# Optimization experiments

Measured on AMD Instinct MI355X. Metric: run time of the kernel, lower is better.

Reference implementation:

```python
import jax, jax.numpy as jnp
import numpy as np

N_NEIGHBORS = 16
NEIGHBOR_LIMIT = 20
N_BINS = 5
EPS = 1e-12


def _distance_matrix(coords):
    # coords: (N, 3) -> (N, N) pairwise Euclidean distances
    sq = jnp.sum(coords * coords, axis=-1)
    dm = sq[:, None] - 2.0 * (coords @ coords.T) + sq[None, :]
    return jnp.sqrt(jnp.abs(dm))


def _shot_lrf(nbh, radius):
    # nbh: (N, K, 3) local neighbor coordinates. SHOT local reference frames.
    d = jnp.linalg.norm(nbh, axis=-1)                       # (N, K)
    w = jnp.maximum(radius - d, 0.0)                        # SHOT distance weights
    cov = jnp.einsum("nk,nki,nkj->nij", w, nbh, nbh)
    cov = cov / (jnp.sum(w, axis=-1)[:, None, None] + EPS)  # (N, 3, 3)
    _, eigvecs = jnp.linalg.eigh(cov)                       # ascending eigenvalues
    x_axes = eigvecs[:, :, 2]                               # largest eigenvalue
    z_axes = eigvecs[:, :, 0]                               # smallest eigenvalue (normal)

    def disambiguate(axes):
        dots = jnp.einsum("nki,ni->nk", nbh, axes)
        pos = jnp.sum((dots >= 0.0).astype(jnp.float32), axis=-1)
        neg = jnp.sum((dots < 0.0).astype(jnp.float32), axis=-1)
        sign = jnp.where(pos >= neg, 1.0, -1.0)
        return axes * sign[:, None]

    x_axes = disambiguate(x_axes)
    z_axes = disambiguate(z_axes)
    y_axes = jnp.cross(z_axes, x_axes)
    return jnp.stack([x_axes, y_axes, z_axes], axis=1)      # (N, 3, 3)


def _log_map(lrfs, nbh):
    # project local neighbors onto tangent plane, preserving vector length
    u = jnp.einsum("nki,ni->nk", nbh, lrfs[:, 0])
    v = jnp.einsum("nki,ni->nk", nbh, lrfs[:, 1])
    plane = jnp.stack([u, v], axis=-1)                      # (N, K, 2)
    norms = jnp.linalg.norm(nbh, axis=-1)
    plane_norms = jnp.linalg.norm(plane, axis=-1)
    return plane * (norms / (plane_norms + EPS))[..., None]


def _histograms(proj, radius, n_bins):
    # proj: (N, K, 2) tangent-plane projections -> (N, n_bins**2) normalized histograms
    step = 2.0 * radius / n_bins
    c = jnp.linspace(-radius, radius, n_bins + 1)[:-1] + step / 2.0
    weights = radius - jnp.sqrt(c[:, None] ** 2 + c[None, :] ** 2)  # (n_bins, n_bins)

    bins = jnp.floor((proj + radius) / step)                # (N, K, 2)
    valid = jnp.all((bins >= 0.0) & (bins < n_bins), axis=-1)
    bx = jnp.clip(bins[..., 0].astype(jnp.int32), 0, n_bins - 1)
    by = jnp.clip(bins[..., 1].astype(jnp.int32), 0, n_bins - 1)
    flat = by * n_bins + bx                                 # hist[row=y_bin, col=x_bin]
    n_pts = flat.shape[0]
    b2 = n_bins * n_bins
    offset = jnp.arange(n_pts)[:, None] * b2
    hist = jnp.zeros((n_pts * b2,), jnp.float32).at[(offset + flat).reshape(-1)].add(
        valid.reshape(-1).astype(jnp.float32))
    hist = hist.reshape(n_pts, n_bins, n_bins) * weights[None]
    hist = hist / jnp.linalg.norm(hist, axis=(1, 2), keepdims=True)
    return hist.reshape(n_pts, b2)


def _single_cloud(coords):
    dm = _distance_matrix(coords)
    order = jnp.argsort(dm, axis=-1)
    dsort = jnp.take_along_axis(dm, order, axis=-1)
    radius = jnp.mean(dsort[:, N_NEIGHBORS])
    nbr_idx = order[:, :NEIGHBOR_LIMIT]
    nbr_dist = dsort[:, :NEIGHBOR_LIMIT]
    nbh = coords[nbr_idx] - coords[:, None, :]              # (N, K, 3) local coords
    fill = (2.0 * radius) / jnp.sqrt(3.0)                   # dummy coord of length 2*radius
    nbh = jnp.where((nbr_dist > radius)[..., None], fill, nbh)
    lrfs = _shot_lrf(nbh, radius)
    proj = _log_map(lrfs, nbh)
    return _histograms(proj, radius, N_BINS)


def setup_inputs() -> dict:
    key = jax.random.key(0)
    batched_coordinates = jax.random.normal(key, (4, 4096, 3), dtype=jnp.float32)
    return {"batched_coordinates": batched_coordinates}


def reference(batched_coordinates):
    return jax.vmap(_single_cloud)(batched_coordinates)
```

## Files before the change

### kernel.cpp

```cpp
#include <hip/hip_runtime.h>
#include <math.h>

#pragma clang fp contract(off)

#define NPTS 4096
#define NBATCH 4
#define NTOT (NBATCH * NPTS)
#define NNB 20
#define NBINS 5
#define LTOP 7

#define SEPS    5.9604644775390625e-8f
#define SSAFMIN 1.17549435e-38f


__device__ __forceinline__ float f_signf(float a, float b) {
  return __builtin_signbit(b) ? -fabsf(a) : fabsf(a);
}

__device__ float slapy2_(float x, float y) {
  float xa = fabsf(x), ya = fabsf(y);
  float w = fmaxf(xa, ya), z = fminf(xa, ya);
  if (z == 0.0f) return w;
  float t = z / w;
  return w * sqrtf(1.0f + t * t);
}

__device__ void slartg_(float f, float g, float* c, float* s, float* r) {
  if (g == 0.0f) {
    *c = 1.0f; *s = 0.0f; *r = f;
  } else if (f == 0.0f) {
    *c = 0.0f; *s = __builtin_signbit(g) ? -1.0f : 1.0f; *r = fabsf(g);
  } else {
    float f1 = fabsf(f);
    float d = sqrtf(f * f + g * g);
    *c = f1 / d;
    float rr = __builtin_signbit(f) ? -d : d;
    *r = rr;
    *s = g / rr;
  }
}

__device__ void slaev2_(float a, float b, float c,
                        float* rt1, float* rt2, float* cs1, float* sn1) {
  float sm = a + c;
  float df = a - c;
  float adf = fabsf(df);
  float tb = b + b;
  float ab = fabsf(tb);
  float acmx, acmn;
  if (fabsf(a) > fabsf(c)) { acmx = a; acmn = c; } else { acmx = c; acmn = a; }
  float rt;
  if (adf > ab)      { float t = ab / adf; rt = adf * sqrtf(1.0f + t * t); }
  else if (adf < ab) { float t = adf / ab; rt = ab * sqrtf(1.0f + t * t); }
  else               { rt = ab * sqrtf(2.0f); }
  int sgn1;
  if (sm < 0.0f) {
    *rt1 = 0.5f * (sm - rt); sgn1 = -1;
    *rt2 = (acmx / *rt1) * acmn - (b / *rt1) * b;
  } else if (sm > 0.0f) {
    *rt1 = 0.5f * (sm + rt); sgn1 = 1;
    *rt2 = (acmx / *rt1) * acmn - (b / *rt1) * b;
  } else {
    *rt1 = 0.5f * rt; *rt2 = -0.5f * rt; sgn1 = 1;
  }
  float cs; int sgn2;
  if (df >= 0.0f) { cs = df + rt; sgn2 = 1; }
  else            { cs = df - rt; sgn2 = -1; }
  float acs = fabsf(cs);
  float csv, snv;
  if (acs > ab) {
    float ct = -tb / cs;
    snv = 1.0f / sqrtf(1.0f + ct * ct);
    csv = ct * snv;
  } else {
    if (ab == 0.0f) { csv = 1.0f; snv = 0.0f; }
    else {
      float tn = -cs / tb;
      csv = 1.0f / sqrtf(1.0f + tn * tn);
      snv = tn * csv;
    }
  }
  if (sgn1 == sgn2) { float tn = csv; csv = -snv; snv = tn; }
  *cs1 = csv; *sn1 = snv;
}

__device__ __forceinline__ float sel3(float a0, float a1, float a2, int i) {
  float r = (i == 1) ? a1 : a0;
  return (i == 2) ? a2 : r;
}
__device__ __forceinline__ float sel2(float a0, float a1, int i) {
  return (i == 1) ? a1 : a0;
}
#define RD(i)   sel3(d0, d1, d2, (i))
#define RE(i)   sel2(e0, e1, (i))
#define RC(i)   sel2(c0r, c1r, (i))
#define RS(i)   sel2(s0r, s1r, (i))
#define WD(i,v) do{ float _t=(v); int _i=(i); d0=(_i==0)?_t:d0; d1=(_i==1)?_t:d1; d2=(_i==2)?_t:d2; }while(0)
#define WE(i,v) do{ float _t=(v); int _i=(i); e0=(_i==0)?_t:e0; e1=(_i==1)?_t:e1; }while(0)
#define WC(i,v) do{ float _t=(v); int _i=(i); c0r=(_i==0)?_t:c0r; c1r=(_i==1)?_t:c1r; }while(0)
#define WS(i,v) do{ float _t=(v); int _i=(i); s0r=(_i==0)?_t:s0r; s1r=(_i==1)?_t:s1r; }while(0)
#define ZROT(ja, jb, cc, ss) do{ int _a=(ja), _b=(jb); float _c=(cc), _s=(ss);                       \
  { float ta=sel3(z00,z01,z02,_a), tb=sel3(z00,z01,z02,_b); float na=_c*ta-_s*tb, nb=_s*ta+_c*tb;   \
    z00=(_a==0)?na:((_b==0)?nb:z00); z01=(_a==1)?na:((_b==1)?nb:z01); z02=(_a==2)?na:((_b==2)?nb:z02);} \
  { float ta=sel3(z10,z11,z12,_a), tb=sel3(z10,z11,z12,_b); float na=_c*ta-_s*tb, nb=_s*ta+_c*tb;   \
    z10=(_a==0)?na:((_b==0)?nb:z10); z11=(_a==1)?na:((_b==1)?nb:z11); z12=(_a==2)?na:((_b==2)?nb:z12);} \
  { float ta=sel3(z20,z21,z22,_a), tb=sel3(z20,z21,z22,_b); float na=_c*ta-_s*tb, nb=_s*ta+_c*tb;   \
    z20=(_a==0)?na:((_b==0)?nb:z20); z21=(_a==1)?na:((_b==1)?nb:z21); z22=(_a==2)?na:((_b==2)?nb:z22);} \
}while(0)
#define ZSWAP(ia, ib) do{ int _a=(ia), _b=(ib);                                                     \
  { float ta=sel3(z00,z01,z02,_a), tb=sel3(z00,z01,z02,_b);                                         \
    z00=(_a==0)?tb:((_b==0)?ta:z00); z01=(_a==1)?tb:((_b==1)?ta:z01); z02=(_a==2)?tb:((_b==2)?ta:z02);} \
  { float ta=sel3(z10,z11,z12,_a), tb=sel3(z10,z11,z12,_b);                                         \
    z10=(_a==0)?tb:((_b==0)?ta:z10); z11=(_a==1)?tb:((_b==1)?ta:z11); z12=(_a==2)?tb:((_b==2)?ta:z12);} \
  { float ta=sel3(z20,z21,z22,_a), tb=sel3(z20,z21,z22,_b);                                         \
    z20=(_a==0)?tb:((_b==0)?ta:z20); z21=(_a==1)?tb:((_b==1)?ta:z21); z22=(_a==2)?tb:((_b==2)?ta:z22);} \
}while(0)

__device__ void eigh3f_reg(float A00, float A10, float A20, float A11, float A21, float A22,
                           float V[3][3]) {
  float taui, v2, beta;
  float alpha = A10;
  float xnorm = fabsf(A20);
  if (xnorm == 0.0f) {
    taui = 0.0f; beta = alpha; v2 = 0.0f;
  } else {
    beta = -f_signf(slapy2_(alpha, xnorm), alpha);
    taui = (beta - alpha) / beta;
    v2 = A20 * (1.0f / (alpha - beta));
  }
  float a11 = A11, a21 = A21, a22 = A22;
  if (taui != 0.0f) {
    float w0 = taui * (a11 + a21 * v2);
    float w1 = taui * (a21 + a22 * v2);
    float al = -0.5f * taui * (w0 + w1 * v2);
    w0 += al; w1 += al * v2;
    a11 -= 2.0f * w0;
    a21 -= (v2 * w0 + w1);
    a22 -= 2.0f * (v2 * w1);
  }
  float d0 = A00, d1 = a11, d2 = a22;
  float e0 = beta, e1 = a21;
  float z00 = 1.0f, z01 = 0.0f, z02 = 0.0f;
  float z10 = 0.0f, z11 = 1.0f, z12 = 0.0f;
  float z20 = 0.0f, z21 = 0.0f, z22 = 1.0f;
  float c0r = 0.0f, c1r = 0.0f, s0r = 0.0f, s1r = 0.0f;

  {
    const int n = 3;
    const float eps = SEPS;
    const float eps2 = SEPS * SEPS;
    const float safmin = SSAFMIN;
    const int nmaxit = 90;
    int jtot = 0;
    int l1 = 1;
    int l = 0, lsv = 0, lend = 0, lendsv = 0, m = 0, mm = 0;
    float p = 0, g = 0, r = 0, c = 0, s = 0, f = 0, bb = 0, rt1 = 0, rt2 = 0;
    float anorm = 0, tst = 0;

L10:
    if (l1 > n) goto L160;
    if (l1 > 1) WE(l1 - 2, 0.0f);
    if (l1 <= n - 1) {
      for (m = l1; m <= n - 1; ++m) {
        tst = fabsf(RE(m - 1));
        if (tst == 0.0f) goto L30;
        if (tst <= (sqrtf(fabsf(RD(m - 1))) * sqrtf(fabsf(RD(m)))) * eps) {
          WE(m - 1, 0.0f);
          goto L30;
        }
      }
    }
    m = n;
L30:
    l = l1; lsv = l; lend = m; lendsv = lend; l1 = m + 1;
    if (lend == l) goto L10;
    anorm = 0.0f;
    for (int i = l; i <= lend; ++i) anorm = fmaxf(anorm, fabsf(RD(i - 1)));
    for (int i = l; i <= lend - 1; ++i) anorm = fmaxf(anorm, fabsf(RE(i - 1)));
    if (anorm == 0.0f) goto L10;
    if (fabsf(RD(lend - 1)) < fabsf(RD(l - 1))) { lend = lsv; l = lendsv; }

    if (lend > l) {
L40:
      if (l != lend) {
        for (m = l; m <= lend - 1; ++m) {
          tst = RE(m - 1) * RE(m - 1);
          if (tst <= (eps2 * fabsf(RD(m - 1))) * fabsf(RD(m)) + safmin) goto L60;
        }
      }
      m = lend;
L60:
      if (m < lend) WE(m - 1, 0.0f);
      p = RD(l - 1);
      if (m == l) goto L80;
      if (m == l + 1) {
        slaev2_(RD(l - 1), RE(l - 1), RD(l), &rt1, &rt2, &c, &s);
        ZROT(l, l - 1, c, s);
        WD(l - 1, rt1); WD(l, rt2); WE(l - 1, 0.0f);
        l += 2;
        if (l <= lend) goto L40;
        goto L140;
      }
      if (jtot == nmaxit) goto L140;
      jtot++;
      g = (RD(l) - p) / (2.0f * RE(l - 1));
      r = slapy2_(g, 1.0f);
      g = RD(m - 1) - p + RE(l - 1) / (g + f_signf(r, g));
      s = 1.0f; c = 1.0f; p = 0.0f;
      for (int i = m - 1; i >= l; --i) {
        f = s * RE(i - 1);
        bb = c * RE(i - 1);
        slartg_(g, f, &c, &s, &r);
        if (i != m - 1) WE(i, r);
        g = RD(i) - p;
        r = (RD(i - 1) - g) * s + 2.0f * c * bb;
        p = s * r;
        WD(i, g + p);
        g = c * r - bb;
        WC(i - 1, c); WS(i - 1, -s);
      }
      mm = m - l + 1;
      for (int j = mm - 1; j >= 1; --j) {
        float ct = RC(l + j - 2), st = RS(l + j - 2);
        ZROT(l + j - 1, l + j - 2, ct, st);
      }
      WD(l - 1, RD(l - 1) - p);
      WE(l - 1, g);
      goto L40;
L80:
      WD(l - 1, p);
      l++;
      if (l <= lend) goto L40;
      goto L140;
    } else {
L90:
      if (l != lend) {
        for (m = l; m >= lend + 1; --m) {
          tst = RE(m - 2) * RE(m - 2);
          if (tst <= (eps2 * fabsf(RD(m - 1))) * fabsf(RD(m - 2)) + safmin) goto L110;
        }
      }
      m = lend;
L110:
      if (m > lend) WE(m - 2, 0.0f);
      p = RD(l - 1);
      if (m == l) goto L130;
      if (m == l - 1) {
        slaev2_(RD(l - 2), RE(l - 2), RD(l - 1), &rt1, &rt2, &c, &s);
        ZROT(l - 1, l - 2, c, s);
        WD(l - 2, rt1); WD(l - 1, rt2); WE(l - 2, 0.0f);
        l -= 2;
        if (l >= lend) goto L90;
        goto L140;
      }
      if (jtot == nmaxit) goto L140;
      jtot++;
      g = (RD(l - 2) - p) / (2.0f * RE(l - 2));
      r = slapy2_(g, 1.0f);
      g = RD(m - 1) - p + RE(l - 2) / (g + f_signf(r, g));
      s = 1.0f; c = 1.0f; p = 0.0f;
      for (int i = m; i <= l - 1; ++i) {
        f = s * RE(i - 1);
        bb = c * RE(i - 1);
        slartg_(g, f, &c, &s, &r);
        if (i != m) WE(i - 2, r);
        g = RD(i - 1) - p;
        r = (RD(i) - g) * s + 2.0f * c * bb;
        p = s * r;
        WD(i - 1, g + p);
        g = c * r - bb;
        WC(i - 1, c); WS(i - 1, s);
      }
      mm = l - m + 1;
      for (int j = 1; j <= mm - 1; ++j) {
        float ct = RC(m + j - 2), st = RS(m + j - 2);
        ZROT(m + j - 1, m + j - 2, ct, st);
      }
      WD(l - 1, RD(l - 1) - p);
      WE(l - 2, g);
      goto L90;
L130:
      WD(l - 1, p);
      l--;
      if (l >= lend) goto L90;
      goto L140;
    }
L140:
    if (jtot < nmaxit) goto L10;
    goto L160;
L160:
    for (int ii = 2; ii <= n; ++ii) {
      int i = ii - 1, k = i;
      float pp = RD(i - 1);
      for (int j = ii; j <= n; ++j)
        if (RD(j - 1) < pp) { k = j; pp = RD(j - 1); }
      if (k != i) {
        WD(k - 1, RD(i - 1));
        WD(i - 1, pp);
        ZSWAP(i - 1, k - 1);
      }
    }
  }

  {
    float t0 = taui * (z10 + v2 * z20);
    float t1 = taui * (z11 + v2 * z21);
    float t2 = taui * (z12 + v2 * z22);
    z10 -= t0; z20 -= t0 * v2;
    z11 -= t1; z21 -= t1 * v2;
    z12 -= t2; z22 -= t2 * v2;
  }
  V[0][0] = z00; V[0][1] = z01; V[0][2] = z02;
  V[1][0] = z10; V[1][1] = z11; V[1][2] = z12;
  V[2][0] = z20; V[2][1] = z21; V[2][2] = z22;
}

__device__ __forceinline__ unsigned wave_min_dpp(unsigned v) {
  unsigned t;
  t = (unsigned)__builtin_amdgcn_update_dpp(-1, (int)v, 0x111, 0xf, 0xf, false); v = t < v ? t : v;
  t = (unsigned)__builtin_amdgcn_update_dpp(-1, (int)v, 0x112, 0xf, 0xf, false); v = t < v ? t : v;
  t = (unsigned)__builtin_amdgcn_update_dpp(-1, (int)v, 0x114, 0xf, 0xf, false); v = t < v ? t : v;
  t = (unsigned)__builtin_amdgcn_update_dpp(-1, (int)v, 0x118, 0xf, 0xf, false); v = t < v ? t : v;
  t = (unsigned)__builtin_amdgcn_update_dpp(-1, (int)v, 0x142, 0xa, 0xf, false); v = t < v ? t : v;
  t = (unsigned)__builtin_amdgcn_update_dpp(-1, (int)v, 0x143, 0xc, 0xf, false); v = t < v ? t : v;
  return v;
}


__global__ __launch_bounds__(1024, 8) void knn_kernel(const float* __restrict__ coords,
                                                      float* __restrict__ nbrD,
                                                      int* __restrict__ nbrI,
                                                      float* __restrict__ d16) {
  __shared__ float4 scs[NPTS];
  int tid = threadIdx.x;
  int wid = tid >> 6;
  int lane = tid & 63;
  int P = blockIdx.x * 16 + wid;
  int b = P >> 12;
  int p = P & (NPTS - 1);
  const float* cb = coords + (size_t)b * NPTS * 3;

  for (int i = tid; i < NPTS; i += 1024) {
    float x = cb[3 * i + 0], y = cb[3 * i + 1], z = cb[3 * i + 2];
    float sq = (x * x + y * y) + z * z;
    scs[i] = make_float4(x, y, z, sq);
  }
  __syncthreads();

  float4 ci = scs[p];
  float xi = ci.x, yi = ci.y, zi = ci.z, sqi = ci.w;

  const double INF = __hiloint2double(0x7FF00000, 0);
  double L[LTOP];
#pragma unroll
  for (int t = 0; t < LTOP; ++t) L[t] = INF;

#pragma unroll 8
  for (int k = 0; k < NPTS / 64; ++k) {
    int j = k * 64 + lane;
    float4 cj = scs[j];
    float dot = (xi * cj.x + yi * cj.y) + zi * cj.z;
    float d2 = (sqi - 2.0f * dot) + cj.w;
    unsigned kb = __float_as_uint(d2) & 0x7FFFFFFFu;
    double cur = __hiloint2double((int)kb, j);
    double m1 = fmax(cur, L[0]);
    double m2 = fmax(cur, L[1]);
    double m3 = fmax(cur, L[2]);
    double m4 = fmax(cur, L[3]);
    double m5 = fmax(cur, L[4]);
    double m6 = fmax(cur, L[5]);
    L[0] = fmin(L[0], cur);
    L[1] = fmin(L[1], m1);
    L[2] = fmin(L[2], m2);
    L[3] = fmin(L[3], m3);
    L[4] = fmin(L[4], m4);
    L[5] = fmin(L[5], m5);
    L[6] = fmin(L[6], m6);
  }

  unsigned resHi = 0, resLo = 0;
  for (int r = 0; r < NNB; ++r) {
    unsigned hi0 = (unsigned)__double2hiint(L[0]);
    unsigned lo0 = (unsigned)__double2loint(L[0]);
    unsigned gh = wave_min_dpp(hi0);
    gh = (unsigned)__builtin_amdgcn_readlane((int)gh, 63);
    unsigned lom = (hi0 == gh) ? lo0 : 0xFFFFFFFFu;
    unsigned gl = wave_min_dpp(lom);
    gl = (unsigned)__builtin_amdgcn_readlane((int)gl, 63);
    bool mine = (hi0 == gh) && (lo0 == gl);
#pragma unroll
    for (int t = 0; t < LTOP - 1; ++t) L[t] = mine ? L[t + 1] : L[t];
    L[LTOP - 1] = mine ? INF : L[LTOP - 1];
    if (lane == r) { resHi = gh; resLo = gl; }
  }

  if (lane < NNB) {
    float dist = sqrtf(__uint_as_float(resHi));
    nbrD[(size_t)lane * NTOT + P] = dist;
    nbrI[(size_t)lane * NTOT + P] = (int)resLo;
    if (lane == 16) d16[P] = dist;
  }
}


__global__ __launch_bounds__(64) void shot_kernel(const float* __restrict__ coords,
                                                  const float* __restrict__ d16,
                                                  const float* __restrict__ nbrD,
                                                  const int* __restrict__ nbrI,
                                                  float* __restrict__ out) {
  __shared__ float buf[NPTS];
  __shared__ float hws[25 * 64];
  int lane = threadIdx.x;
  int g = blockIdx.x * 64 + lane;
  int b = g >> 12;
  int p = g & (NPTS - 1);
  const float* cb = coords + (size_t)b * NPTS * 3;

  for (int i = lane; i < NPTS; i += 64) buf[i] = d16[(size_t)b * NPTS + i];

  int jj[NNB];
  float dd[NNB];
#pragma unroll
  for (int k = 0; k < NNB; ++k) {
    jj[k] = nbrI[(size_t)k * NTOT + g];
    dd[k] = nbrD[(size_t)k * NTOT + g];
  }
  float gx[NNB], gy[NNB], gz[NNB];
#pragma unroll
  for (int k = 0; k < NNB; ++k) {
    int j = jj[k];
    gx[k] = cb[j * 3 + 0];
    gy[k] = cb[j * 3 + 1];
    gz[k] = cb[j * 3 + 2];
  }
  float xi = cb[p * 3 + 0], yi = cb[p * 3 + 1], zi = cb[p * 3 + 2];

  __syncthreads();
  float s = 0.0f;
  for (int k = 0; k < NPTS; ++k) s += buf[k];
  float radius = s / 4096.0f;

  float fill = 2.0f * radius / sqrtf(3.0f);

  float nbx[NNB], nby[NNB], nbz[NNB], dk[NNB];
#pragma unroll
  for (int k = 0; k < NNB; ++k) {
    float nx, ny, nz;
    if (dd[k] > radius) { nx = fill; ny = fill; nz = fill; }
    else {
      nx = gx[k] - xi;
      ny = gy[k] - yi;
      nz = gz[k] - zi;
    }
    nbx[k] = nx; nby[k] = ny; nbz[k] = nz;
    dk[k] = sqrtf((nx * nx + ny * ny) + nz * nz);
  }

  float wsum = 0.0f;
  float c00 = 0, c11 = 0, c22 = 0;
  float c01 = 0, c10 = 0, c02 = 0, c20 = 0, c12 = 0, c21 = 0;
  for (int k = 0; k < NNB; ++k) {
    float w = fmaxf(radius - dk[k], 0.0f);
    wsum += w;
    float wx = w * nbx[k], wy = w * nby[k], wz = w * nbz[k];
    c00 += wx * nbx[k]; c01 += wx * nby[k]; c02 += wx * nbz[k];
    c10 += wy * nbx[k]; c11 += wy * nby[k]; c12 += wy * nbz[k];
    c20 += wz * nbx[k]; c21 += wz * nby[k]; c22 += wz * nbz[k];
  }
  float den = wsum + 1e-12f;
  float a00 = c00 / den, a11 = c11 / den, a22 = c22 / den;
  float a01 = c01 / den, a10 = c10 / den;
  float a02 = c02 / den, a20 = c20 / den;
  float a12 = c12 / den, a21 = c21 / den;
  float A10 = 0.5f * (a01 + a10);
  float A20 = 0.5f * (a02 + a20);
  float A21 = 0.5f * (a12 + a21);

  float V[3][3];
  eigh3f_reg(a00, A10, A20, a11, A21, a22, V);

  float xax0 = V[0][2], xax1 = V[1][2], xax2 = V[2][2];
  float zax0 = V[0][0], zax1 = V[1][0], zax2 = V[2][0];

  {
    int pos = 0, neg = 0;
    for (int k = 0; k < NNB; ++k) {
      float dt = (nbx[k] * xax0 + nby[k] * xax1) + nbz[k] * xax2;
      if (dt >= 0.0f) pos++; else neg++;
    }
    if (pos < neg) { xax0 = -xax0; xax1 = -xax1; xax2 = -xax2; }
  }
  {
    int pos = 0, neg = 0;
    for (int k = 0; k < NNB; ++k) {
      float dt = (nbx[k] * zax0 + nby[k] * zax1) + nbz[k] * zax2;
      if (dt >= 0.0f) pos++; else neg++;
    }
    if (pos < neg) { zax0 = -zax0; zax1 = -zax1; zax2 = -zax2; }
  }
  float yax0 = zax1 * xax2 - zax2 * xax1;
  float yax1 = zax2 * xax0 - zax0 * xax2;
  float yax2 = zax0 * xax1 - zax1 * xax0;

  float* hh = &hws[lane];
#pragma unroll
  for (int k = 0; k < NBINS * NBINS; ++k) hh[k * 64] = 0.0f;
  float stp = 2.0f * radius / (float)NBINS;
  for (int k = 0; k < NNB; ++k) {
    float u = (nbx[k] * xax0 + nby[k] * xax1) + nbz[k] * xax2;
    float v = (nbx[k] * yax0 + nby[k] * yax1) + nbz[k] * yax2;
    float pn = sqrtf(u * u + v * v);
    float sc = dk[k] / (pn + 1e-12f);
    float pu = u * sc, pv = v * sc;
    float bxf = floorf((pu + radius) / stp);
    float byf = floorf((pv + radius) / stp);
    if (bxf >= 0.0f && bxf < (float)NBINS && byf >= 0.0f && byf < (float)NBINS) {
      int bx = (int)bxf, by = (int)byf;
      hh[(by * NBINS + bx) * 64] += 1.0f;
    }
  }
  float cvals[NBINS];
#pragma unroll
  for (int i = 0; i < NBINS; ++i) cvals[i] = ((float)i * stp - radius) + 0.5f * stp;
  float nrm2 = 0.0f;
  float hreg[NBINS * NBINS];
#pragma unroll
  for (int i = 0; i < NBINS; ++i) {
#pragma unroll
    for (int j = 0; j < NBINS; ++j) {
      float wgt = radius - sqrtf(cvals[i] * cvals[i] + cvals[j] * cvals[j]);
      float h = hh[(i * NBINS + j) * 64] * wgt;
      hreg[i * NBINS + j] = h;
      nrm2 += h * h;
    }
  }
  float nrm = sqrtf(nrm2);
#pragma unroll
  for (int k = 0; k < NBINS * NBINS; ++k) {
    out[(size_t)g * (NBINS * NBINS) + k] = hreg[k] / nrm;
  }
}


extern "C" void kernel_launch(void* const* d_in, const int* in_sizes, int n_in,
                              void* d_out, int out_size, void* d_ws, size_t ws_size,
                              hipStream_t stream) {
  const float* coords = (const float*)d_in[0];
  float* out = (float*)d_out;

  float* wsf = (float*)d_ws;
  float* d16 = wsf + 8;
  float* nbrD = wsf + 8 + (size_t)NTOT;
  int* nbrI = (int*)(nbrD + (size_t)NNB * NTOT);

  knn_kernel<<<NTOT / 16, 1024, 0, stream>>>(coords, nbrD, nbrI, d16);
  shot_kernel<<<NTOT / 64, 64, 0, stream>>>(coords, d16, nbrD, nbrI, out);
}
```

Before: 116.0 us.

## Split radius reduction into its own kernel and shrink SHOT blocks to 8 threads

Before, every 64-thread shot block reloaded all 4096 d16 values and summed them serially to get the radius. That sum now runs once per batch in a separate small kernel, and the shot kernel just reads the result. The shot kernel also drops to 8 threads per block, giving 2048 blocks to spread across CUs, and neighbour coordinates are loaded only when the neighbour lies within the radius. In exchange there is an extra launch, the radius kernel is a serial sum run by only four blocks, and blocks of 8 threads leave wavefronts mostly empty.

New measurement: 139.2 us. +20.0%, slower.

```diff
diff --git a/kernel.cpp b/kernel.cpp
--- a/kernel.cpp
+++ b/kernel.cpp
@@ -9,6 +9,7 @@
 #define NNB 20
 #define NBINS 5
 #define LTOP 7
+#define SPB 8
 
 #define SEPS    5.9604644775390625e-8f
 #define SSAFMIN 1.17549435e-38f
@@ -404,20 +405,31 @@
 }
 
 
-__global__ __launch_bounds__(64) void shot_kernel(const float* __restrict__ coords,
-                                                  const float* __restrict__ d16,
-                                                  const float* __restrict__ nbrD,
-                                                  const int* __restrict__ nbrI,
-                                                  float* __restrict__ out) {
+__global__ __launch_bounds__(64) void radius_kernel(const float* __restrict__ d16,
+                                                    float* __restrict__ radius) {
   __shared__ float buf[NPTS];
-  __shared__ float hws[25 * 64];
+  int b = blockIdx.x;
   int lane = threadIdx.x;
-  int g = blockIdx.x * 64 + lane;
+  for (int i = lane; i < NPTS; i += 64) buf[i] = d16[(size_t)b * NPTS + i];
+  __syncthreads();
+  float s = 0.0f;
+  for (int k = 0; k < NPTS; ++k) s += buf[k];
+  if (lane == 0) radius[b] = s / 4096.0f;
+}
+
+
+__global__ __launch_bounds__(SPB) void shot_kernel(const float* __restrict__ coords,
+                                                   const float* __restrict__ radius_arr,
+                                                   const float* __restrict__ nbrD,
+                                                   const int* __restrict__ nbrI,
+                                                   float* __restrict__ out) {
+  __shared__ float hws[25 * SPB];
+  int lane = threadIdx.x;
+  int g = blockIdx.x * SPB + lane;
   int b = g >> 12;
   int p = g & (NPTS - 1);
   const float* cb = coords + (size_t)b * NPTS * 3;
-
-  for (int i = lane; i < NPTS; i += 64) buf[i] = d16[(size_t)b * NPTS + i];
+  float radius = radius_arr[b];
 
   int jj[NNB];
   float dd[NNB];
@@ -426,32 +438,19 @@
     jj[k] = nbrI[(size_t)k * NTOT + g];
     dd[k] = nbrD[(size_t)k * NTOT + g];
   }
-  float gx[NNB], gy[NNB], gz[NNB];
+  float xi = cb[p * 3 + 0], yi = cb[p * 3 + 1], zi = cb[p * 3 + 2];
+  float fill = 2.0f * radius / sqrtf(3.0f);
+
+  float nbx[NNB], nby[NNB], nbz[NNB], dk[NNB];
 #pragma unroll
   for (int k = 0; k < NNB; ++k) {
     int j = jj[k];
-    gx[k] = cb[j * 3 + 0];
-    gy[k] = cb[j * 3 + 1];
-    gz[k] = cb[j * 3 + 2];
-  }
-  float xi = cb[p * 3 + 0], yi = cb[p * 3 + 1], zi = cb[p * 3 + 2];
-
-  __syncthreads();
-  float s = 0.0f;
-  for (int k = 0; k < NPTS; ++k) s += buf[k];
-  float radius = s / 4096.0f;
-
-  float fill = 2.0f * radius / sqrtf(3.0f);
-
-  float nbx[NNB], nby[NNB], nbz[NNB], dk[NNB];
-#pragma unroll
-  for (int k = 0; k < NNB; ++k) {
     float nx, ny, nz;
     if (dd[k] > radius) { nx = fill; ny = fill; nz = fill; }
     else {
-      nx = gx[k] - xi;
-      ny = gy[k] - yi;
-      nz = gz[k] - zi;
+      nx = cb[j * 3 + 0] - xi;
+      ny = cb[j * 3 + 1] - yi;
+      nz = cb[j * 3 + 2] - zi;
     }
     nbx[k] = nx; nby[k] = ny; nbz[k] = nz;
     dk[k] = sqrtf((nx * nx + ny * ny) + nz * nz);
@@ -505,7 +504,7 @@
 
   float* hh = &hws[lane];
 #pragma unroll
-  for (int k = 0; k < NBINS * NBINS; ++k) hh[k * 64] = 0.0f;
+  for (int k = 0; k < NBINS * NBINS; ++k) hh[k * SPB] = 0.0f;
   float stp = 2.0f * radius / (float)NBINS;
   for (int k = 0; k < NNB; ++k) {
     float u = (nbx[k] * xax0 + nby[k] * xax1) + nbz[k] * xax2;
@@ -517,7 +516,7 @@
     float byf = floorf((pv + radius) / stp);
     if (bxf >= 0.0f && bxf < (float)NBINS && byf >= 0.0f && byf < (float)NBINS) {
       int bx = (int)bxf, by = (int)byf;
-      hh[(by * NBINS + bx) * 64] += 1.0f;
+      hh[(by * NBINS + bx) * SPB] += 1.0f;
     }
   }
   float cvals[NBINS];
@@ -530,7 +529,7 @@
 #pragma unroll
     for (int j = 0; j < NBINS; ++j) {
       float wgt = radius - sqrtf(cvals[i] * cvals[i] + cvals[j] * cvals[j]);
-      float h = hh[(i * NBINS + j) * 64] * wgt;
+      float h = hh[(i * NBINS + j) * SPB] * wgt;
       hreg[i * NBINS + j] = h;
       nrm2 += h * h;
     }
@@ -550,10 +549,12 @@
   float* out = (float*)d_out;
 
   float* wsf = (float*)d_ws;
+  float* radius = wsf;
   float* d16 = wsf + 8;
   float* nbrD = wsf + 8 + (size_t)NTOT;
   int* nbrI = (int*)(nbrD + (size_t)NNB * NTOT);
 
   knn_kernel<<<NTOT / 16, 1024, 0, stream>>>(coords, nbrD, nbrI, d16);
-  shot_kernel<<<NTOT / 64, 64, 0, stream>>>(coords, d16, nbrD, nbrI, out);
-}
+  radius_kernel<<<NBATCH, 64, 0, stream>>>(d16, radius);
+  shot_kernel<<<NTOT / SPB, SPB, 0, stream>>>(coords, radius, nbrD, nbrI, out);
+}
```
